# Kernel tuning notes

Hardware: AMD Instinct MI355X
Metric: run time of the kernel (lower is better)

## Reference

```python
import jax, jax.numpy as jnp
import numpy as np

VOCAB = 30
EMBED = 512   # must equal HIDDEN: h0 = embed[b,0,:]
HIDDEN = 512
CLASSES = 2
B, T = 512, 256


def setup_inputs() -> dict:
    key = jax.random.key(0)
    ks = jax.random.split(key, 8)
    # tokens in [1, VOCAB) so 0 is reserved for padding
    x = jax.random.randint(ks[0], (B, T), 1, VOCAB)
    # ragged lengths: zero-pad each row after a random length in [T//2, T]
    lengths = jax.random.randint(ks[1], (B,), T // 2, T + 1)
    pos = jnp.arange(T)[None, :]
    x = jnp.where(pos < lengths[:, None], x, 0).astype(jnp.int64)
    s_e = 1.0 / np.sqrt(HIDDEN)
    embed_table = jax.random.normal(ks[2], (VOCAB, EMBED), jnp.float32) * 0.02
    w_ih = jax.random.uniform(ks[3], (3 * HIDDEN, EMBED), jnp.float32, -s_e, s_e)
    w_hh = jax.random.uniform(ks[4], (3 * HIDDEN, HIDDEN), jnp.float32, -s_e, s_e)
    b_ih = jax.random.uniform(ks[5], (3 * HIDDEN,), jnp.float32, -s_e, s_e)
    b_hh = jax.random.uniform(ks[6], (3 * HIDDEN,), jnp.float32, -s_e, s_e)
    fc_w = jax.random.uniform(ks[7], (CLASSES, HIDDEN), jnp.float32, -s_e, s_e)
    fc_b = jnp.zeros((CLASSES,), jnp.float32)
    return {"x": x, "embed_table": embed_table, "w_ih": w_ih, "w_hh": w_hh,
            "b_ih": b_ih, "b_hh": b_hh, "fc_w": fc_w, "fc_b": fc_b}


def reference(x, embed_table, w_ih, w_hh, b_ih, b_hh, fc_w, fc_b):
    emb = embed_table[x]                      # [B, T, E]
    h0 = emb[:, 0, :]                         # initial hidden = embedding of token 0
    # valid at step i (i>=1) iff no zero token among positions 1..i (break semantics)
    zero = (x[:, 1:] == 0).astype(jnp.int32)  # [B, T-1]
    valid = jnp.cumsum(zero, axis=1) == 0     # [B, T-1]

    def step(h, inp):
        e_t, v_t = inp                        # [B, E], [B]
        gi = e_t @ w_ih.T + b_ih              # [B, 3H]
        gh = h @ w_hh.T + b_hh                # [B, 3H]
        i_r, i_z, i_n = jnp.split(gi, 3, axis=-1)
        h_r, h_z, h_n = jnp.split(gh, 3, axis=-1)
        r = jax.nn.sigmoid(i_r + h_r)
        z = jax.nn.sigmoid(i_z + h_z)
        n = jnp.tanh(i_n + r * h_n)
        h_new = (1.0 - z) * n + z * h
        h = jnp.where(v_t[:, None], h_new, h)
        return h, None

    xs = (jnp.swapaxes(emb[:, 1:, :], 0, 1), valid.T)   # time-major
    h_final, _ = jax.lax.scan(step, h0, xs)
    logits = h_final @ fc_w.T + fc_b          # [B, CLASSES]
    return logits
```

## Files before the change

kernel.cpp:

```cpp
#include <hip/hip_runtime.h>
#include <stdint.h>

#define BB 512
#define TT 256
#define HH 512
#define G3 1536
#define NVOC 30

#define GROUPS 32
#define BT 16
#define JBL 8
#define JT 64
#define NBLK 256

typedef float f32x4 __attribute__((ext_vector_type(4)));
typedef short s16x8 __attribute__((ext_vector_type(8)));
typedef unsigned int u32;
typedef unsigned long long u64;

__device__ __forceinline__ unsigned short f2bf(float f) {
    unsigned u = __float_as_uint(f);
    u = u + 0x7FFFu + ((u >> 16) & 1u);
    return (unsigned short)(u >> 16);
}
__device__ __forceinline__ float bf2f(unsigned short s) {
    return __uint_as_float(((unsigned)s) << 16);
}
__device__ __forceinline__ float sigm(float x) { return 1.f / (1.f + __expf(-x)); }
__device__ __forceinline__ float tanh_fast(float x) {
    x = fminf(15.f, fmaxf(-15.f, x));
    float e = __expf(2.f * x);
    return (e - 1.f) / (e + 1.f);
}

__global__ void k_wconv(const float* __restrict__ w, unsigned short* __restrict__ wbf, int n) {
    int i = blockIdx.x * blockDim.x + threadIdx.x;
    if (i < n) wbf[i] = f2bf(w[i]);
}

__global__ void k_gitab(const float* __restrict__ embed, const float* __restrict__ w_ih,
                        const float* __restrict__ b_ih, const float* __restrict__ b_hh,
                        float* __restrict__ gi) {
    int id = blockIdx.x * blockDim.x + threadIdx.x;
    if (id >= NVOC * G3) return;
    int v = id / G3, g = id - v * G3;
    float s = b_ih[g] + (g < 2 * HH ? b_hh[g] : 0.f);
    const float* er = embed + (size_t)v * HH;
    const float* wr = w_ih + (size_t)g * HH;
    #pragma unroll 8
    for (int k = 0; k < HH; ++k) s += er[k] * wr[k];
    gi[id] = s;
}

__global__ void k_init(const int* __restrict__ x32, const float* __restrict__ embed,
                       u32* __restrict__ h_pk, int* __restrict__ lastvalid) {
    int b = blockIdx.x, lane = threadIdx.x;
    int is64 = (x32[1] == 0) ? 1 : 0;
    int xv0 = x32[(b * TT) << is64];
    for (int k = lane; k < HH; k += 64) {
        float e = embed[(size_t)xv0 * HH + k];
        unsigned short hi = f2bf(e);
        unsigned short lo = f2bf(e - bf2f(hi));
        u32 pk = ((u32)hi << 16) | (u32)(lo & 0xFFFC);
        h_pk[(size_t)b * HH + k] = pk;
        h_pk[(size_t)BB * HH + (size_t)b * HH + k] = pk | 2u;
    }
    int m = TT;
    for (int t = 1 + lane; t < TT; t += 64)
        if (x32[(b * TT + t) << is64] == 0) m = min(m, t);
    #pragma unroll
    for (int off = 32; off; off >>= 1) m = min(m, __shfl_xor(m, off));
    if (lane == 0) lastvalid[b] = m - 1;
}

__global__ void __launch_bounds__(256, 1)
k_main(const int* __restrict__ x32, const unsigned short* __restrict__ wbf,
       const float* __restrict__ gi_table, const float* __restrict__ b_hh,
       u32* __restrict__ h_pk, const int* __restrict__ lastvalid, int* __restrict__ flags) {
    __shared__ unsigned short h_hi[BT * HH];
    __shared__ unsigned short h_lo[BT * HH];
    __shared__ char lds_pad[56 * 1024];
    if (threadIdx.x == 0) ((volatile char*)lds_pad)[0] = 0;

    const int blk = blockIdx.x;
    const int xcd = blk & 7, s = blk >> 3;
    const int group = xcd * 4 + (s >> 3);
    const int jb = s & 7;
    const int b0 = group * BT;
    const int tid = threadIdx.x;
    const int wave = tid >> 6, lane = tid & 63;
    const int l16 = lane & 15, lq = lane >> 4;
    const int jc = jb * JT + wave * 16 + l16;
    const int kb16 = lq * 8;
    const int is64 = (x32[1] == 0) ? 1 : 0;

    s16x8 wreg[3][16];
    #pragma unroll
    for (int g = 0; g < 3; ++g)
        #pragma unroll
        for (int c = 0; c < 16; ++c)
            wreg[g][c] = *reinterpret_cast<const s16x8*>(
                wbf + (size_t)(g * HH + jc) * HH + c * 32 + kb16);
    #pragma unroll
    for (int g = 0; g < 3; ++g)
        #pragma unroll
        for (int c = 0; c < 16; ++c)
            asm volatile("" : "+v"(wreg[g][c]));

    float bhn = b_hh[2 * HH + jc];
    asm volatile("" : "+v"(bhn));
    int lv[4]; float hp[4];
    #pragma unroll
    for (int i = 0; i < 4; ++i) {
        int row = b0 + lq * 4 + i;
        lv[i] = lastvalid[row];
        asm volatile("" : "+v"(lv[i]));
        u32 p = h_pk[(size_t)row * HH + jc];
        hp[i] = bf2f((unsigned short)(p >> 16)) + bf2f((unsigned short)(p & 0xFFFC));
    }
    int gmax = 0;
    for (int r = 0; r < BT; ++r) gmax = max(gmax, lastvalid[b0 + r]);

    int* myflag = flags + group * JBL + jb;
    int* fbase = flags + group * JBL;
    u32* hbuf0 = h_pk;
    u32* hbuf1 = h_pk + (size_t)BB * HH;

    for (int t = 1; t <= gmax; ++t) {
        const u32 tg = (u32)((t - 1) & 3);
        const u32 tgpair = tg | (tg << 2);

        u32* rslot = ((t - 1) & 1) ? hbuf1 : hbuf0;
        u64* src = reinterpret_cast<u64*>(rslot + (size_t)b0 * HH);
        u64 vals[16];
        #pragma unroll
        for (int u = 0; u < 16; ++u)
            vals[u] = __hip_atomic_load(src + (size_t)u * 256 + tid,
                                        __ATOMIC_RELAXED, __HIP_MEMORY_SCOPE_AGENT);

        int xv[4]; float gr[4], gz[4], gn[4];
        #pragma unroll
        for (int i = 0; i < 4; ++i) {
            int row = b0 + lq * 4 + i;
            xv[i] = x32[((row * TT) + t) << is64];
        }
        #pragma unroll
        for (int i = 0; i < 4; ++i) {
            const float* gt = gi_table + (size_t)xv[i] * G3;
            gr[i] = gt[jc]; gz[i] = gt[HH + jc]; gn[i] = gt[2 * HH + jc];
        }

        u32 bad = 0;
        #pragma unroll
        for (int u = 0; u < 16; ++u) {
            u32 p0 = (u32)vals[u], p1 = (u32)(vals[u] >> 32);
            u32 tags = (p0 & 3u) | ((p1 & 3u) << 2);
            if (tags != tgpair) bad |= (1u << u);
        }
        int guard = 0;
        while (__any(bad != 0)) {
            #pragma unroll
            for (int u = 0; u < 16; ++u) {
                if (bad & (1u << u)) {
                    u64 v = __hip_atomic_load(src + (size_t)u * 256 + tid,
                                              __ATOMIC_RELAXED, __HIP_MEMORY_SCOPE_AGENT);
                    u32 p0 = (u32)v, p1 = (u32)(v >> 32);
                    if (((p0 & 3u) | ((p1 & 3u) << 2)) == tgpair) {
                        vals[u] = v; bad &= ~(1u << u);
                    }
                }
            }
            if (++guard > (1 << 15)) break;
        }

        {
            u32* hi32 = reinterpret_cast<u32*>(h_hi);
            u32* lo32 = reinterpret_cast<u32*>(h_lo);
            #pragma unroll
            for (int u = 0; u < 16; ++u) {
                u32 p0 = (u32)vals[u], p1 = (u32)(vals[u] >> 32);
                int idx = u * 256 + (tid ^ ((u & 15) << 2));
                hi32[idx] = (p1 & 0xFFFF0000u) | (p0 >> 16);
                lo32[idx] = (((p1 & 0xFFFFu) << 16) | (p0 & 0xFFFFu)) & 0xFFFCFFFCu;
            }
        }
        __syncthreads();
        asm volatile("s_waitcnt vmcnt(0)" ::: "memory");
        if (tid == 0)
            __hip_atomic_store(myflag, t, __ATOMIC_RELAXED, __HIP_MEMORY_SCOPE_AGENT);

        f32x4 a0h = {0.f,0.f,0.f,0.f}, a0l = a0h, a1h = a0h, a1l = a0h, a2h = a0h, a2l = a0h;
        const int rowbase = l16 * HH;
        #pragma unroll
        for (int c = 0; c < 16; ++c) {
            int off = rowbase + ((kb16 + c * 32) ^ (l16 << 3));
            s16x8 ahi = *reinterpret_cast<const s16x8*>(h_hi + off);
            s16x8 alo = *reinterpret_cast<const s16x8*>(h_lo + off);
            a0h = __builtin_amdgcn_mfma_f32_16x16x32_bf16(ahi, wreg[0][c], a0h, 0, 0, 0);
            a1h = __builtin_amdgcn_mfma_f32_16x16x32_bf16(ahi, wreg[1][c], a1h, 0, 0, 0);
            a2h = __builtin_amdgcn_mfma_f32_16x16x32_bf16(ahi, wreg[2][c], a2h, 0, 0, 0);
            a0l = __builtin_amdgcn_mfma_f32_16x16x32_bf16(alo, wreg[0][c], a0l, 0, 0, 0);
            a1l = __builtin_amdgcn_mfma_f32_16x16x32_bf16(alo, wreg[1][c], a1l, 0, 0, 0);
            a2l = __builtin_amdgcn_mfma_f32_16x16x32_bf16(alo, wreg[2][c], a2l, 0, 0, 0);
        }
        f32x4 s0 = a0h + a0l, s1 = a1h + a1l, s2 = a2h + a2l;

        {
            const int want = t - 1;
            int guard2 = 0;
            for (;;) {
                int f = 0x7fffffff;
                if (lane < JBL)
                    f = __hip_atomic_load(fbase + lane, __ATOMIC_RELAXED,
                                          __HIP_MEMORY_SCOPE_AGENT);
                if (__all(f >= want)) break;
                __builtin_amdgcn_s_sleep(1);
                if (++guard2 > (1 << 17)) break;
            }
        }

        const u32 tgs = (u32)(t & 3);
        u32* dst = (t & 1) ? hbuf1 : hbuf0;
        #pragma unroll
        for (int i = 0; i < 4; ++i) {
            int row = b0 + lq * 4 + i;
            float r = sigm(s0[i] + gr[i]);
            float z = sigm(s1[i] + gz[i]);
            float n = tanh_fast(gn[i] + r * (s2[i] + bhn));
            float hnew = (1.f - z) * n + z * hp[i];
            float hout = (t <= lv[i]) ? hnew : hp[i];
            hp[i] = hout;
            unsigned short hi = f2bf(hout);
            unsigned short lo = f2bf(hout - bf2f(hi));
            u32 pk = ((u32)hi << 16) | (u32)(lo & 0xFFFC) | tgs;
            __hip_atomic_store(dst + (size_t)row * HH + jc, pk,
                               __ATOMIC_RELAXED, __HIP_MEMORY_SCOPE_AGENT);
        }
        __syncthreads();
    }
}

__global__ void k_logits(const u32* __restrict__ h_pk, const int* __restrict__ lastvalid,
                         const float* __restrict__ fc_w, const float* __restrict__ fc_b,
                         float* __restrict__ out) {
    int wave = threadIdx.x >> 6, lane = threadIdx.x & 63;
    int row = blockIdx.x * 4 + wave;
    if (row >= BB) return;
    int g0 = (row / BT) * BT;
    int gmax = 0;
    for (int r = 0; r < BT; ++r) gmax = max(gmax, lastvalid[g0 + r]);
    const u32* hf = h_pk + (size_t)(gmax & 1) * BB * HH + (size_t)row * HH;
    float d0 = 0.f, d1 = 0.f;
    int k = lane * 8;
    #pragma unroll
    for (int u = 0; u < 8; ++u) {
        u32 p = hf[k + u];
        float hv = bf2f((unsigned short)(p >> 16)) + bf2f((unsigned short)(p & 0xFFFC));
        d0 += hv * fc_w[k + u];
        d1 += hv * fc_w[HH + k + u];
    }
    #pragma unroll
    for (int off = 32; off; off >>= 1) {
        d0 += __shfl_xor(d0, off);
        d1 += __shfl_xor(d1, off);
    }
    if (lane == 0) {
        out[row * 2 + 0] = d0 + fc_b[0];
        out[row * 2 + 1] = d1 + fc_b[1];
    }
}

extern "C" void kernel_launch(void* const* d_in, const int* in_sizes, int n_in,
                              void* d_out, int out_size, void* d_ws, size_t ws_size,
                              hipStream_t stream) {
    const int*   x32   = (const int*)d_in[0];
    const float* embed = (const float*)d_in[1];
    const float* w_ih  = (const float*)d_in[2];
    const float* w_hh  = (const float*)d_in[3];
    const float* b_ih  = (const float*)d_in[4];
    const float* b_hh  = (const float*)d_in[5];
    const float* fc_w  = (const float*)d_in[6];
    const float* fc_b  = (const float*)d_in[7];
    float* out = (float*)d_out;

    char* ws = (char*)d_ws;
    unsigned short* wbf = (unsigned short*)ws;
    u32* h_pk           = (u32*)(ws + 1572864);
    float* gi_table     = (float*)(ws + 3670016);
    int* lastvalid      = (int*)(ws + 3854336);
    int* flags          = (int*)(ws + 3856384);

    hipMemsetAsync(flags, 0, NBLK * sizeof(int), stream);
    k_wconv<<<(G3 * HH + 255) / 256, 256, 0, stream>>>(w_hh, wbf, G3 * HH);
    k_gitab<<<(NVOC * G3 + 255) / 256, 256, 0, stream>>>(embed, w_ih, b_ih, b_hh, gi_table);
    k_init<<<BB, 64, 0, stream>>>(x32, embed, h_pk, lastvalid);
    k_main<<<NBLK, 256, 0, stream>>>(x32, wbf, gi_table, b_hh, h_pk, lastvalid, flags);
    k_logits<<<BB / 4, 256, 0, stream>>>(h_pk, lastvalid, fc_w, fc_b, out);
}
```

Measured before the change: 1.319 ms.

## Process two batch groups per block, halving grid to 128 blocks

Each k_main block now owns two 16-row batch groups instead of one, with separate LDS buffers for each. Per step it loads, converts and multiplies both groups against the same register-resident weights, and keeps separate flags and barriers per group. This halves the number of resident blocks and doubles per-block serial work per timestep. The aim is probably to reduce how many blocks take part in cross-block synchronization, at the cost of a longer critical path per step and more register pressure.

Result: slower. 2.984 ms (+126.3%).

```diff
diff --git a/kernel.cpp b/kernel.cpp
--- a/kernel.cpp
+++ b/kernel.cpp
@@ -11,7 +11,8 @@
 #define BT 16
 #define JBL 8
 #define JT 64
-#define NBLK 256
+#define NBLK 128
+#define NTHR 256
 
 typedef float f32x4 __attribute__((ext_vector_type(4)));
 typedef short s16x8 __attribute__((ext_vector_type(8)));
@@ -73,20 +74,22 @@
     if (lane == 0) lastvalid[b] = m - 1;
 }
 
-__global__ void __launch_bounds__(256, 1)
+__global__ void __launch_bounds__(NTHR, 1)
 k_main(const int* __restrict__ x32, const unsigned short* __restrict__ wbf,
        const float* __restrict__ gi_table, const float* __restrict__ b_hh,
        u32* __restrict__ h_pk, const int* __restrict__ lastvalid, int* __restrict__ flags) {
-    __shared__ unsigned short h_hi[BT * HH];
-    __shared__ unsigned short h_lo[BT * HH];
-    __shared__ char lds_pad[56 * 1024];
+    __shared__ unsigned short hA_hi[BT * HH];
+    __shared__ unsigned short hA_lo[BT * HH];
+    __shared__ unsigned short hB_hi[BT * HH];
+    __shared__ unsigned short hB_lo[BT * HH];
+    __shared__ char lds_pad[24 * 1024];
     if (threadIdx.x == 0) ((volatile char*)lds_pad)[0] = 0;
 
     const int blk = blockIdx.x;
-    const int xcd = blk & 7, s = blk >> 3;
-    const int group = xcd * 4 + (s >> 3);
-    const int jb = s & 7;
-    const int b0 = group * BT;
+    const int jb = blk & 7;
+    const int gpair = blk >> 3;
+    const int gA = gpair * 2, gB = gpair * 2 + 1;
+    const int b0A = gA * BT, b0B = gB * BT;
     const int tid = threadIdx.x;
     const int wave = tid >> 6, lane = tid & 63;
     const int l16 = lane & 15, lq = lane >> 4;
@@ -109,73 +112,79 @@
 
     float bhn = b_hh[2 * HH + jc];
     asm volatile("" : "+v"(bhn));
-    int lv[4]; float hp[4];
+    int lvA[4], lvB[4]; float hpA[4], hpB[4];
     #pragma unroll
     for (int i = 0; i < 4; ++i) {
-        int row = b0 + lq * 4 + i;
-        lv[i] = lastvalid[row];
-        asm volatile("" : "+v"(lv[i]));
-        u32 p = h_pk[(size_t)row * HH + jc];
-        hp[i] = bf2f((unsigned short)(p >> 16)) + bf2f((unsigned short)(p & 0xFFFC));
-    }
-    int gmax = 0;
-    for (int r = 0; r < BT; ++r) gmax = max(gmax, lastvalid[b0 + r]);
-
-    int* myflag = flags + group * JBL + jb;
-    int* fbase = flags + group * JBL;
+        int rA = b0A + lq * 4 + i, rB = b0B + lq * 4 + i;
+        lvA[i] = lastvalid[rA]; lvB[i] = lastvalid[rB];
+        asm volatile("" : "+v"(lvA[i])); asm volatile("" : "+v"(lvB[i]));
+        u32 pA = h_pk[(size_t)rA * HH + jc], pB = h_pk[(size_t)rB * HH + jc];
+        hpA[i] = bf2f((unsigned short)(pA >> 16)) + bf2f((unsigned short)(pA & 0xFFFC));
+        hpB[i] = bf2f((unsigned short)(pB >> 16)) + bf2f((unsigned short)(pB & 0xFFFC));
+    }
+    int gmaxA = 0, gmaxB = 0;
+    for (int r = 0; r < BT; ++r) {
+        gmaxA = max(gmaxA, lastvalid[b0A + r]);
+        gmaxB = max(gmaxB, lastvalid[b0B + r]);
+    }
+    const int gmax = max(gmaxA, gmaxB);
+
+    int* myflagA = flags + gA * JBL + jb;
+    int* myflagB = flags + gB * JBL + jb;
+    int* fbaseA = flags + gA * JBL;
+    int* fbaseB = flags + gB * JBL;
     u32* hbuf0 = h_pk;
     u32* hbuf1 = h_pk + (size_t)BB * HH;
 
     for (int t = 1; t <= gmax; ++t) {
         const u32 tg = (u32)((t - 1) & 3);
         const u32 tgpair = tg | (tg << 2);
-
         u32* rslot = ((t - 1) & 1) ? hbuf1 : hbuf0;
-        u64* src = reinterpret_cast<u64*>(rslot + (size_t)b0 * HH);
-        u64 vals[16];
-        #pragma unroll
-        for (int u = 0; u < 16; ++u)
-            vals[u] = __hip_atomic_load(src + (size_t)u * 256 + tid,
-                                        __ATOMIC_RELAXED, __HIP_MEMORY_SCOPE_AGENT);
-
-        int xv[4]; float gr[4], gz[4], gn[4];
-        #pragma unroll
-        for (int i = 0; i < 4; ++i) {
-            int row = b0 + lq * 4 + i;
-            xv[i] = x32[((row * TT) + t) << is64];
-        }
-        #pragma unroll
-        for (int i = 0; i < 4; ++i) {
-            const float* gt = gi_table + (size_t)xv[i] * G3;
-            gr[i] = gt[jc]; gz[i] = gt[HH + jc]; gn[i] = gt[2 * HH + jc];
-        }
-
-        u32 bad = 0;
-        #pragma unroll
-        for (int u = 0; u < 16; ++u) {
-            u32 p0 = (u32)vals[u], p1 = (u32)(vals[u] >> 32);
-            u32 tags = (p0 & 3u) | ((p1 & 3u) << 2);
-            if (tags != tgpair) bad |= (1u << u);
-        }
-        int guard = 0;
-        while (__any(bad != 0)) {
+        u32* dst = (t & 1) ? hbuf1 : hbuf0;
+        const u32 tgs = (u32)(t & 3);
+        const int doA = (t <= gmaxA), doB = (t <= gmaxB);
+
+        int xvA[4], xvB[4];
+        float grA[4], gzA[4], gnA[4], grB[4], gzB[4], gnB[4];
+
+        if (doA) {
+            u64* src = reinterpret_cast<u64*>(rslot + (size_t)b0A * HH);
+            u64 vals[16];
+            #pragma unroll
+            for (int u = 0; u < 16; ++u)
+                vals[u] = __hip_atomic_load(src + (size_t)u * 256 + tid,
+                                            __ATOMIC_RELAXED, __HIP_MEMORY_SCOPE_AGENT);
+            #pragma unroll
+            for (int i = 0; i < 4; ++i)
+                xvA[i] = x32[(((b0A + lq * 4 + i) * TT) + t) << is64];
+            #pragma unroll
+            for (int i = 0; i < 4; ++i) {
+                const float* gt = gi_table + (size_t)xvA[i] * G3;
+                grA[i] = gt[jc]; gzA[i] = gt[HH + jc]; gnA[i] = gt[2 * HH + jc];
+            }
+            u32 bad = 0;
             #pragma unroll
             for (int u = 0; u < 16; ++u) {
-                if (bad & (1u << u)) {
-                    u64 v = __hip_atomic_load(src + (size_t)u * 256 + tid,
-                                              __ATOMIC_RELAXED, __HIP_MEMORY_SCOPE_AGENT);
-                    u32 p0 = (u32)v, p1 = (u32)(v >> 32);
-                    if (((p0 & 3u) | ((p1 & 3u) << 2)) == tgpair) {
-                        vals[u] = v; bad &= ~(1u << u);
+                u32 p0 = (u32)vals[u], p1 = (u32)(vals[u] >> 32);
+                if (((p0 & 3u) | ((p1 & 3u) << 2)) != tgpair) bad |= (1u << u);
+            }
+            int guard = 0;
+            while (__any(bad != 0)) {
+                #pragma unroll
+                for (int u = 0; u < 16; ++u) {
+                    if (bad & (1u << u)) {
+                        u64 v = __hip_atomic_load(src + (size_t)u * 256 + tid,
+                                                  __ATOMIC_RELAXED, __HIP_MEMORY_SCOPE_AGENT);
+                        u32 p0 = (u32)v, p1 = (u32)(v >> 32);
+                        if (((p0 & 3u) | ((p1 & 3u) << 2)) == tgpair) {
+                            vals[u] = v; bad &= ~(1u << u);
+                        }
                     }
                 }
-            }
-            if (++guard > (1 << 15)) break;
-        }
-
-        {
-            u32* hi32 = reinterpret_cast<u32*>(h_hi);
-            u32* lo32 = reinterpret_cast<u32*>(h_lo);
+                if (++guard > (1 << 15)) break;
+            }
+            u32* hi32 = reinterpret_cast<u32*>(hA_hi);
+            u32* lo32 = reinterpret_cast<u32*>(hA_lo);
             #pragma unroll
             for (int u = 0; u < 16; ++u) {
                 u32 p0 = (u32)vals[u], p1 = (u32)(vals[u] >> 32);
@@ -184,58 +193,151 @@
                 lo32[idx] = (((p1 & 0xFFFFu) << 16) | (p0 & 0xFFFFu)) & 0xFFFCFFFCu;
             }
         }
+
+        if (doB) {
+            u64* src = reinterpret_cast<u64*>(rslot + (size_t)b0B * HH);
+            u64 vals[16];
+            #pragma unroll
+            for (int u = 0; u < 16; ++u)
+                vals[u] = __hip_atomic_load(src + (size_t)u * 256 + tid,
+                                            __ATOMIC_RELAXED, __HIP_MEMORY_SCOPE_AGENT);
+            #pragma unroll
+            for (int i = 0; i < 4; ++i)
+                xvB[i] = x32[(((b0B + lq * 4 + i) * TT) + t) << is64];
+            #pragma unroll
+            for (int i = 0; i < 4; ++i) {
+                const float* gt = gi_table + (size_t)xvB[i] * G3;
+                grB[i] = gt[jc]; gzB[i] = gt[HH + jc]; gnB[i] = gt[2 * HH + jc];
+            }
+            u32 bad = 0;
+            #pragma unroll
+            for (int u = 0; u < 16; ++u) {
+                u32 p0 = (u32)vals[u], p1 = (u32)(vals[u] >> 32);
+                if (((p0 & 3u) | ((p1 & 3u) << 2)) != tgpair) bad |= (1u << u);
+            }
+            int guard = 0;
+            while (__any(bad != 0)) {
+                #pragma unroll
+                for (int u = 0; u < 16; ++u) {
+                    if (bad & (1u << u)) {
+                        u64 v = __hip_atomic_load(src + (size_t)u * 256 + tid,
+                                                  __ATOMIC_RELAXED, __HIP_MEMORY_SCOPE_AGENT);
+                        u32 p0 = (u32)v, p1 = (u32)(v >> 32);
+                        if (((p0 & 3u) | ((p1 & 3u) << 2)) == tgpair) {
+                            vals[u] = v; bad &= ~(1u << u);
+                        }
+                    }
+                }
+                if (++guard > (1 << 15)) break;
+            }
+            u32* hi32 = reinterpret_cast<u32*>(hB_hi);
+            u32* lo32 = reinterpret_cast<u32*>(hB_lo);
+            #pragma unroll
+            for (int u = 0; u < 16; ++u) {
+                u32 p0 = (u32)vals[u], p1 = (u32)(vals[u] >> 32);
+                int idx = u * 256 + (tid ^ ((u & 15) << 2));
+                hi32[idx] = (p1 & 0xFFFF0000u) | (p0 >> 16);
+                lo32[idx] = (((p1 & 0xFFFFu) << 16) | (p0 & 0xFFFFu)) & 0xFFFCFFFCu;
+            }
+        }
+
         __syncthreads();
         asm volatile("s_waitcnt vmcnt(0)" ::: "memory");
-        if (tid == 0)
-            __hip_atomic_store(myflag, t, __ATOMIC_RELAXED, __HIP_MEMORY_SCOPE_AGENT);
-
-        f32x4 a0h = {0.f,0.f,0.f,0.f}, a0l = a0h, a1h = a0h, a1l = a0h, a2h = a0h, a2l = a0h;
+        if (tid == 0) {
+            if (doA) __hip_atomic_store(myflagA, t, __ATOMIC_RELAXED, __HIP_MEMORY_SCOPE_AGENT);
+            if (doB) __hip_atomic_store(myflagB, t, __ATOMIC_RELAXED, __HIP_MEMORY_SCOPE_AGENT);
+        }
+
         const int rowbase = l16 * HH;
-        #pragma unroll
-        for (int c = 0; c < 16; ++c) {
-            int off = rowbase + ((kb16 + c * 32) ^ (l16 << 3));
-            s16x8 ahi = *reinterpret_cast<const s16x8*>(h_hi + off);
-            s16x8 alo = *reinterpret_cast<const s16x8*>(h_lo + off);
-            a0h = __builtin_amdgcn_mfma_f32_16x16x32_bf16(ahi, wreg[0][c], a0h, 0, 0, 0);
-            a1h = __builtin_amdgcn_mfma_f32_16x16x32_bf16(ahi, wreg[1][c], a1h, 0, 0, 0);
-            a2h = __builtin_amdgcn_mfma_f32_16x16x32_bf16(ahi, wreg[2][c], a2h, 0, 0, 0);
-            a0l = __builtin_amdgcn_mfma_f32_16x16x32_bf16(alo, wreg[0][c], a0l, 0, 0, 0);
-            a1l = __builtin_amdgcn_mfma_f32_16x16x32_bf16(alo, wreg[1][c], a1l, 0, 0, 0);
-            a2l = __builtin_amdgcn_mfma_f32_16x16x32_bf16(alo, wreg[2][c], a2l, 0, 0, 0);
+
+        if (doA) {
+            f32x4 a0h = {0.f,0.f,0.f,0.f}, a0l = a0h, a1h = a0h, a1l = a0h, a2h = a0h, a2l = a0h;
+            #pragma unroll
+            for (int c = 0; c < 16; ++c) {
+                int off = rowbase + ((kb16 + c * 32) ^ (l16 << 3));
+                s16x8 ahi = *reinterpret_cast<const s16x8*>(hA_hi + off);
+                s16x8 alo = *reinterpret_cast<const s16x8*>(hA_lo + off);
+                a0h = __builtin_amdgcn_mfma_f32_16x16x32_bf16(ahi, wreg[0][c], a0h, 0, 0, 0);
+                a1h = __builtin_amdgcn_mfma_f32_16x16x32_bf16(ahi, wreg[1][c], a1h, 0, 0, 0);
+                a2h = __builtin_amdgcn_mfma_f32_16x16x32_bf16(ahi, wreg[2][c], a2h, 0, 0, 0);
+                a0l = __builtin_amdgcn_mfma_f32_16x16x32_bf16(alo, wreg[0][c], a0l, 0, 0, 0);
+                a1l = __builtin_amdgcn_mfma_f32_16x16x32_bf16(alo, wreg[1][c], a1l, 0, 0, 0);
+                a2l = __builtin_amdgcn_mfma_f32_16x16x32_bf16(alo, wreg[2][c], a2l, 0, 0, 0);
+            }
+            f32x4 s0 = a0h + a0l, s1 = a1h + a1l, s2 = a2h + a2l;
+            {
+                const int want = t - 1; int guard2 = 0;
+                for (;;) {
+                    int f = 0x7fffffff;
+                    if (lane < JBL)
+                        f = __hip_atomic_load(fbaseA + lane, __ATOMIC_RELAXED,
+                                              __HIP_MEMORY_SCOPE_AGENT);
+                    if (__all(f >= want)) break;
+                    __builtin_amdgcn_s_sleep(1);
+                    if (++guard2 > (1 << 17)) break;
+                }
+            }
+            #pragma unroll
+            for (int i = 0; i < 4; ++i) {
+                int row = b0A + lq * 4 + i;
+                float r = sigm(s0[i] + grA[i]);
+                float z = sigm(s1[i] + gzA[i]);
+                float n = tanh_fast(gnA[i] + r * (s2[i] + bhn));
+                float hnew = (1.f - z) * n + z * hpA[i];
+                float hout = (t <= lvA[i]) ? hnew : hpA[i];
+                hpA[i] = hout;
+                unsigned short hi = f2bf(hout);
+                unsigned short lo = f2bf(hout - bf2f(hi));
+                u32 pk = ((u32)hi << 16) | (u32)(lo & 0xFFFC) | tgs;
+                __hip_atomic_store(dst + (size_t)row * HH + jc, pk,
+                                   __ATOMIC_RELAXED, __HIP_MEMORY_SCOPE_AGENT);
+            }
         }
-        f32x4 s0 = a0h + a0l, s1 = a1h + a1l, s2 = a2h + a2l;
-
-        {
-            const int want = t - 1;
-            int guard2 = 0;
-            for (;;) {
-                int f = 0x7fffffff;
-                if (lane < JBL)
-                    f = __hip_atomic_load(fbase + lane, __ATOMIC_RELAXED,
-                                          __HIP_MEMORY_SCOPE_AGENT);
-                if (__all(f >= want)) break;
-                __builtin_amdgcn_s_sleep(1);
-                if (++guard2 > (1 << 17)) break;
+
+        if (doB) {
+            f32x4 a0h = {0.f,0.f,0.f,0.f}, a0l = a0h, a1h = a0h, a1l = a0h, a2h = a0h, a2l = a0h;
+            #pragma unroll
+            for (int c = 0; c < 16; ++c) {
+                int off = rowbase + ((kb16 + c * 32) ^ (l16 << 3));
+                s16x8 ahi = *reinterpret_cast<const s16x8*>(hB_hi + off);
+                s16x8 alo = *reinterpret_cast<const s16x8*>(hB_lo + off);
+                a0h = __builtin_amdgcn_mfma_f32_16x16x32_bf16(ahi, wreg[0][c], a0h, 0, 0, 0);
+                a1h = __builtin_amdgcn_mfma_f32_16x16x32_bf16(ahi, wreg[1][c], a1h, 0, 0, 0);
+                a2h = __builtin_amdgcn_mfma_f32_16x16x32_bf16(ahi, wreg[2][c], a2h, 0, 0, 0);
+                a0l = __builtin_amdgcn_mfma_f32_16x16x32_bf16(alo, wreg[0][c], a0l, 0, 0, 0);
+                a1l = __builtin_amdgcn_mfma_f32_16x16x32_bf16(alo, wreg[1][c], a1l, 0, 0, 0);
+                a2l = __builtin_amdgcn_mfma_f32_16x16x32_bf16(alo, wreg[2][c], a2l, 0, 0, 0);
+            }
+            f32x4 s0 = a0h + a0l, s1 = a1h + a1l, s2 = a2h + a2l;
+            {
+                const int want = t - 1; int guard2 = 0;
+                for (;;) {
+                    int f = 0x7fffffff;
+                    if (lane < JBL)
+                        f = __hip_atomic_load(fbaseB + lane, __ATOMIC_RELAXED,
+                                              __HIP_MEMORY_SCOPE_AGENT);
+                    if (__all(f >= want)) break;
+                    __builtin_amdgcn_s_sleep(1);
+                    if (++guard2 > (1 << 17)) break;
+                }
+            }
+            #pragma unroll
+            for (int i = 0; i < 4; ++i) {
+                int row = b0B + lq * 4 + i;
+                float r = sigm(s0[i] + grB[i]);
+                float z = sigm(s1[i] + gzB[i]);
+                float n = tanh_fast(gnB[i] + r * (s2[i] + bhn));
+                float hnew = (1.f - z) * n + z * hpB[i];
+                float hout = (t <= lvB[i]) ? hnew : hpB[i];
+                hpB[i] = hout;
+                unsigned short hi = f2bf(hout);
+                unsigned short lo = f2bf(hout - bf2f(hi));
+                u32 pk = ((u32)hi << 16) | (u32)(lo & 0xFFFC) | tgs;
+                __hip_atomic_store(dst + (size_t)row * HH + jc, pk,
+                                   __ATOMIC_RELAXED, __HIP_MEMORY_SCOPE_AGENT);
             }
         }
 
-        const u32 tgs = (u32)(t & 3);
-        u32* dst = (t & 1) ? hbuf1 : hbuf0;
-        #pragma unroll
-        for (int i = 0; i < 4; ++i) {
-            int row = b0 + lq * 4 + i;
-            float r = sigm(s0[i] + gr[i]);
-            float z = sigm(s1[i] + gz[i]);
-            float n = tanh_fast(gn[i] + r * (s2[i] + bhn));
-            float hnew = (1.f - z) * n + z * hp[i];
-            float hout = (t <= lv[i]) ? hnew : hp[i];
-            hp[i] = hout;
-            unsigned short hi = f2bf(hout);
-            unsigned short lo = f2bf(hout - bf2f(hi));
-            u32 pk = ((u32)hi << 16) | (u32)(lo & 0xFFFC) | tgs;
-            __hip_atomic_store(dst + (size_t)row * HH + jc, pk,
-                               __ATOMIC_RELAXED, __HIP_MEMORY_SCOPE_AGENT);
-        }
         __syncthreads();
     }
 }
@@ -290,10 +392,10 @@
     int* lastvalid      = (int*)(ws + 3854336);
     int* flags          = (int*)(ws + 3856384);
 
-    hipMemsetAsync(flags, 0, NBLK * sizeof(int), stream);
+    hipMemsetAsync(flags, 0, GROUPS * JBL * sizeof(int), stream);
     k_wconv<<<(G3 * HH + 255) / 256, 256, 0, stream>>>(w_hh, wbf, G3 * HH);
     k_gitab<<<(NVOC * G3 + 255) / 256, 256, 0, stream>>>(embed, w_ih, b_ih, b_hh, gi_table);
     k_init<<<BB, 64, 0, stream>>>(x32, embed, h_pk, lastvalid);
-    k_main<<<NBLK, 256, 0, stream>>>(x32, wbf, gi_table, b_hh, h_pk, lastvalid, flags);
+    k_main<<<NBLK, NTHR, 0, stream>>>(x32, wbf, gi_table, b_hh, h_pk, lastvalid, flags);
     k_logits<<<BB / 4, 256, 0, stream>>>(h_pk, lastvalid, fc_w, fc_b, out);
 }
```

## Feed MFMA operands directly from global loads, dropping LDS staging of hidden state

Applied to the files above, without the earlier changes.

Each wave now loads its own MFMA A-operand fragments of the previous hidden state straight from global memory into registers, in a 4-deep rolling prefetch. Tag checks and spin-retries happen per k-chunk instead of over a block-wide staged tile. This removes the LDS write/read round trip and one of the two block barriers per timestep, so the MFMAs can start as soon as the first chunks arrive. The cost is more global traffic, since each of the four waves reloads the same 16 rows. The completion flag is also published only after the whole matmul, which may delay the other blocks that wait on it.

New measurement: 2.418 ms. 83.4% more time.

```diff
diff --git a/kernel.cpp b/kernel.cpp
--- a/kernel.cpp
+++ b/kernel.cpp
@@ -77,9 +77,7 @@
 k_main(const int* __restrict__ x32, const unsigned short* __restrict__ wbf,
        const float* __restrict__ gi_table, const float* __restrict__ b_hh,
        u32* __restrict__ h_pk, const int* __restrict__ lastvalid, int* __restrict__ flags) {
-    __shared__ unsigned short h_hi[BT * HH];
-    __shared__ unsigned short h_lo[BT * HH];
-    __shared__ char lds_pad[56 * 1024];
+    __shared__ char lds_pad[88 * 1024];
     if (threadIdx.x == 0) ((volatile char*)lds_pad)[0] = 0;
 
     const int blk = blockIdx.x;
@@ -128,15 +126,8 @@
 
     for (int t = 1; t <= gmax; ++t) {
         const u32 tg = (u32)((t - 1) & 3);
-        const u32 tgpair = tg | (tg << 2);
-
         u32* rslot = ((t - 1) & 1) ? hbuf1 : hbuf0;
-        u64* src = reinterpret_cast<u64*>(rslot + (size_t)b0 * HH);
-        u64 vals[16];
-        #pragma unroll
-        for (int u = 0; u < 16; ++u)
-            vals[u] = __hip_atomic_load(src + (size_t)u * 256 + tid,
-                                        __ATOMIC_RELAXED, __HIP_MEMORY_SCOPE_AGENT);
+        u64* srcw = reinterpret_cast<u64*>(rslot) + ((size_t)(b0 + l16) * 256 + lq * 4);
 
         int xv[4]; float gr[4], gz[4], gn[4];
         #pragma unroll
@@ -150,60 +141,66 @@
             gr[i] = gt[jc]; gz[i] = gt[HH + jc]; gn[i] = gt[2 * HH + jc];
         }
 
-        u32 bad = 0;
-        #pragma unroll
-        for (int u = 0; u < 16; ++u) {
-            u32 p0 = (u32)vals[u], p1 = (u32)(vals[u] >> 32);
-            u32 tags = (p0 & 3u) | ((p1 & 3u) << 2);
-            if (tags != tgpair) bad |= (1u << u);
-        }
-        int guard = 0;
-        while (__any(bad != 0)) {
+        f32x4 a0h = {0.f,0.f,0.f,0.f}, a0l = a0h, a1h = a0h, a1l = a0h, a2h = a0h, a2l = a0h;
+        u64 vb[4][4];
+        #pragma unroll
+        for (int w = 0; w < 4; ++w)
             #pragma unroll
-            for (int u = 0; u < 16; ++u) {
-                if (bad & (1u << u)) {
-                    u64 v = __hip_atomic_load(src + (size_t)u * 256 + tid,
-                                              __ATOMIC_RELAXED, __HIP_MEMORY_SCOPE_AGENT);
-                    u32 p0 = (u32)v, p1 = (u32)(v >> 32);
-                    if (((p0 & 3u) | ((p1 & 3u) << 2)) == tgpair) {
-                        vals[u] = v; bad &= ~(1u << u);
+            for (int j = 0; j < 4; ++j)
+                vb[w][j] = __hip_atomic_load(srcw + (size_t)w * 16 + j,
+                                             __ATOMIC_RELAXED, __HIP_MEMORY_SCOPE_AGENT);
+        #pragma unroll
+        for (int c = 0; c < 16; ++c) {
+            const int wsel = c & 3;
+            u32 bad = 0;
+            #pragma unroll
+            for (int j = 0; j < 4; ++j) {
+                u32 p0 = (u32)vb[wsel][j], p1 = (u32)(vb[wsel][j] >> 32);
+                if (((p0 & 3u) != tg) | ((p1 & 3u) != tg)) bad |= (1u << j);
+            }
+            int guard = 0;
+            while (__any(bad != 0)) {
+                #pragma unroll
+                for (int j = 0; j < 4; ++j) {
+                    if (bad & (1u << j)) {
+                        u64 v = __hip_atomic_load(srcw + (size_t)c * 16 + j,
+                                                  __ATOMIC_RELAXED, __HIP_MEMORY_SCOPE_AGENT);
+                        u32 p0 = (u32)v, p1 = (u32)(v >> 32);
+                        if (((p0 & 3u) == tg) & ((p1 & 3u) == tg)) {
+                            vb[wsel][j] = v; bad &= ~(1u << j);
+                        }
                     }
                 }
-            }
-            if (++guard > (1 << 15)) break;
-        }
-
-        {
-            u32* hi32 = reinterpret_cast<u32*>(h_hi);
-            u32* lo32 = reinterpret_cast<u32*>(h_lo);
+                if (++guard > (1 << 15)) break;
+            }
+            s16x8 ahi, alo;
             #pragma unroll
-            for (int u = 0; u < 16; ++u) {
-                u32 p0 = (u32)vals[u], p1 = (u32)(vals[u] >> 32);
-                int idx = u * 256 + (tid ^ ((u & 15) << 2));
-                hi32[idx] = (p1 & 0xFFFF0000u) | (p0 >> 16);
-                lo32[idx] = (((p1 & 0xFFFFu) << 16) | (p0 & 0xFFFFu)) & 0xFFFCFFFCu;
-            }
-        }
-        __syncthreads();
-        asm volatile("s_waitcnt vmcnt(0)" ::: "memory");
-        if (tid == 0)
-            __hip_atomic_store(myflag, t, __ATOMIC_RELAXED, __HIP_MEMORY_SCOPE_AGENT);
-
-        f32x4 a0h = {0.f,0.f,0.f,0.f}, a0l = a0h, a1h = a0h, a1l = a0h, a2h = a0h, a2l = a0h;
-        const int rowbase = l16 * HH;
-        #pragma unroll
-        for (int c = 0; c < 16; ++c) {
-            int off = rowbase + ((kb16 + c * 32) ^ (l16 << 3));
-            s16x8 ahi = *reinterpret_cast<const s16x8*>(h_hi + off);
-            s16x8 alo = *reinterpret_cast<const s16x8*>(h_lo + off);
+            for (int j = 0; j < 4; ++j) {
+                u32 p0 = (u32)vb[wsel][j], p1 = (u32)(vb[wsel][j] >> 32);
+                ahi[2 * j]     = (short)(p0 >> 16);
+                ahi[2 * j + 1] = (short)(p1 >> 16);
+                alo[2 * j]     = (short)(p0 & 0xFFFC);
+                alo[2 * j + 1] = (short)(p1 & 0xFFFC);
+            }
             a0h = __builtin_amdgcn_mfma_f32_16x16x32_bf16(ahi, wreg[0][c], a0h, 0, 0, 0);
             a1h = __builtin_amdgcn_mfma_f32_16x16x32_bf16(ahi, wreg[1][c], a1h, 0, 0, 0);
             a2h = __builtin_amdgcn_mfma_f32_16x16x32_bf16(ahi, wreg[2][c], a2h, 0, 0, 0);
             a0l = __builtin_amdgcn_mfma_f32_16x16x32_bf16(alo, wreg[0][c], a0l, 0, 0, 0);
             a1l = __builtin_amdgcn_mfma_f32_16x16x32_bf16(alo, wreg[1][c], a1l, 0, 0, 0);
             a2l = __builtin_amdgcn_mfma_f32_16x16x32_bf16(alo, wreg[2][c], a2l, 0, 0, 0);
+            if (c < 12) {
+                #pragma unroll
+                for (int j = 0; j < 4; ++j)
+                    vb[wsel][j] = __hip_atomic_load(srcw + (size_t)(c + 4) * 16 + j,
+                                                    __ATOMIC_RELAXED, __HIP_MEMORY_SCOPE_AGENT);
+            }
         }
         f32x4 s0 = a0h + a0l, s1 = a1h + a1l, s2 = a2h + a2l;
+
+        asm volatile("s_waitcnt vmcnt(0)" ::: "memory");
+        __syncthreads();
+        if (tid == 0)
+            __hip_atomic_store(myflag, t, __ATOMIC_RELAXED, __HIP_MEMORY_SCOPE_AGENT);
 
         {
             const int want = t - 1;
@@ -236,7 +233,6 @@
             __hip_atomic_store(dst + (size_t)row * HH + jc, pk,
                                __ATOMIC_RELAXED, __HIP_MEMORY_SCOPE_AGENT);
         }
-        __syncthreads();
     }
 }
 
```
